# Optimization experiments

Hardware: AMD Instinct MI355X
Metric: run time of the kernel (lower is better)

## Reference

```python
import jax, jax.numpy as jnp
import numpy as np

VOCAB = 128000
HID = 256
SEQ = 512

def setup_inputs() -> dict:
    key = jax.random.key(0)
    k1, k2, k3, k4 = jax.random.split(key, 4)
    input_question = jax.random.randint(k1, (SEQ,), 0, VOCAB, dtype=jnp.int32)
    emb = jax.random.normal(k2, (VOCAB, HID), dtype=jnp.float32) * 0.02
    # torch Linear(2H, H): weight [H, 2H], bias [H]
    W = jax.random.normal(k3, (HID, 2 * HID), dtype=jnp.float32) * (1.0 / np.sqrt(2 * HID))
    b = jax.random.normal(k4, (HID,), dtype=jnp.float32) * 0.01
    return {"input_question": input_question, "emb": emb, "W": W, "b": b}

def reference(input_question, emb, W, b):
    # gather all word embeddings up-front: [S, H]
    xs = emb[input_question]
    # split W into hidden part and input part so each step is two small GEMVs
    Wh = W[:, :HID]   # acts on hidden_state (first in concat)
    Wx = W[:, HID:]   # acts on embedded word
    # precompute input contribution for all steps: [S, H]
    inp = xs @ Wx.T + b

    def step(h, inp_t):
        h_new = jnp.tanh(h @ Wh.T + inp_t)
        return h_new, None

    h0 = jnp.zeros((HID,), dtype=emb.dtype)
    h_final, _ = jax.lax.scan(step, h0, inp)
    return h_final
```

## Files before the change

### kernel.cpp

```cpp
#include <hip/hip_runtime.h>
#include <math.h>

#define HID 256
#define SEQ 512

typedef float v4f __attribute__((ext_vector_type(4)));

__global__ __launch_bounds__(256) void qrnn_phase1(
    const int* __restrict__ idx, const float* __restrict__ emb,
    const float* __restrict__ W, const float* __restrict__ b,
    float* __restrict__ inp)
{
    const int t = blockIdx.x;
    const int i = threadIdx.x;
    __shared__ float xs[HID];
    const size_t row = (size_t)idx[t];
    xs[i] = emb[row * HID + i];
    __syncthreads();

    const float* wr = W + (size_t)i * (2 * HID) + HID;
    float acc = b[i];
#pragma unroll
    for (int k = 0; k < HID / 4; ++k) {
        const float4 w4 = *reinterpret_cast<const float4*>(wr + k * 4);
        const float4 x4 = *reinterpret_cast<const float4*>(&xs[k * 4]);
        acc = fmaf(w4.x, x4.x, acc);
        acc = fmaf(w4.y, x4.y, acc);
        acc = fmaf(w4.z, x4.z, acc);
        acc = fmaf(w4.w, x4.w, acc);
    }
    inp[t * HID + i] = acc;
}

template <int CTRL>
__device__ __forceinline__ float dpp_add(float v)
{
    int x = __builtin_amdgcn_update_dpp(0, __float_as_int(v), CTRL, 0xF, 0xF, true);
    return v + __int_as_float(x);
}

#define PIN8(a) asm volatile("" : "+v"(a[0]), "+v"(a[1]), "+v"(a[2]), \
                                  "+v"(a[3]), "+v"(a[4]), "+v"(a[5]), \
                                  "+v"(a[6]), "+v"(a[7]))

__global__ __launch_bounds__(512, 2) void qrnn_phase2(
    const float* __restrict__ W, const float* __restrict__ inp,
    float* __restrict__ out)
{
    const int tid = threadIdx.x;
    const int r = tid & 7;
    const int g = tid >> 3;
    const int m_out = r & 3;
    const int i_out = 4 * g + m_out;

    __shared__ float hbuf[2][HID];

    if (tid < HID) hbuf[0][tid] = 0.0f;

    v4f wv[4][8];
#pragma unroll
    for (int m = 0; m < 4; ++m) {
        const float* wrow = W + (size_t)(4 * g + m) * (2 * HID) + r * 32;
#pragma unroll
        for (int k = 0; k < 8; ++k)
            wv[m][k] = *reinterpret_cast<const v4f*>(wrow + k * 4);
    }
    PIN8(wv[0]); PIN8(wv[1]); PIN8(wv[2]); PIN8(wv[3]);

    float ip = inp[i_out];
    float h = 0.0f;
    __syncthreads();

    auto step = [&](const float* __restrict__ src, float* __restrict__ dst,
                    int tnext) {
        v4f h4[8];
#pragma unroll
        for (int k = 0; k < 8; ++k)
            h4[k] = *reinterpret_cast<const v4f*>(src + r * 32 + (((k ^ r) & 7) << 2));

        float ip_next = inp[(tnext & (SEQ - 1)) * HID + i_out];

        float acc[4];
#pragma unroll
        for (int m = 0; m < 4; ++m) {
            float a = 0.0f;
#pragma unroll
            for (int k = 0; k < 8; ++k) {
                a = fmaf(wv[m][k].x, h4[k].x, a);
                a = fmaf(wv[m][k].y, h4[k].y, a);
                a = fmaf(wv[m][k].z, h4[k].z, a);
                a = fmaf(wv[m][k].w, h4[k].w, a);
            }
            acc[m] = a;
        }

#pragma unroll
        for (int m = 0; m < 4; ++m) {
            acc[m] = dpp_add<0xB1>(acc[m]);
            acc[m] = dpp_add<0x4E>(acc[m]);
            acc[m] = dpp_add<0x141>(acc[m]);
        }

        float s0 = (r & 1) ? acc[1] : acc[0];
        float s1 = (r & 1) ? acc[3] : acc[2];
        float d  = (r & 2) ? s1 : s0;

        d += ip;
        float e = __expf(2.0f * d);
        h = 1.0f - 2.0f / (e + 1.0f);

        if (r < 4)
            dst[i_out ^ (((i_out >> 5) & 7) << 2)] = h;

        ip = ip_next;
        __syncthreads();
    };

#pragma unroll 1
    for (int t = 0; t < SEQ; t += 2) {
        step(&hbuf[0][0], &hbuf[1][0], t + 1);
        step(&hbuf[1][0], &hbuf[0][0], t + 2);
    }

    if (r < 4) out[i_out] = h;
}

extern "C" void kernel_launch(void* const* d_in, const int* in_sizes, int n_in,
                              void* d_out, int out_size, void* d_ws, size_t ws_size,
                              hipStream_t stream)
{
    const int*   idx = (const int*)d_in[0];
    const float* emb = (const float*)d_in[1];
    const float* W   = (const float*)d_in[2];
    const float* b   = (const float*)d_in[3];
    float* out = (float*)d_out;
    float* inp = (float*)d_ws;

    qrnn_phase1<<<SEQ, HID, 0, stream>>>(idx, emb, W, b, inp);
    qrnn_phase2<<<1, 512, 0, stream>>>(W, inp, out);
}
```

Baseline: 281.2 us.

## Repartition recurrent GEMV to 16 lanes per 8 rows with butterfly reduce-scatter

Phase 2 now assigns 16 lanes to each group of 8 output rows, so each lane covers 16 columns instead of 32. The cross-lane reduction becomes a recursive-halving reduce-scatter using DPP moves with select-based give/keep, which replaces the full all-reduce on every accumulator. The goal is to shorten the serial FMA chain and cut DPP/add work per step on the sequential critical path. In exchange it adds row-rotate DPP controls and more select logic, and drops the minimum-blocks hint in favour of a waves_per_eu attribute.

```diff
diff --git a/kernel.cpp b/kernel.cpp
--- a/kernel.cpp
+++ b/kernel.cpp
@@ -33,39 +33,49 @@
 }
 
 template <int CTRL>
-__device__ __forceinline__ float dpp_add(float v)
+__device__ __forceinline__ float dpp_mov(float v)
 {
-    int x = __builtin_amdgcn_update_dpp(0, __float_as_int(v), CTRL, 0xF, 0xF, true);
-    return v + __int_as_float(x);
+    return __int_as_float(
+        __builtin_amdgcn_update_dpp(0, __float_as_int(v), CTRL, 0xF, 0xF, true));
 }
 
-#define PIN8(a) asm volatile("" : "+v"(a[0]), "+v"(a[1]), "+v"(a[2]), \
-                                  "+v"(a[3]), "+v"(a[4]), "+v"(a[5]), \
-                                  "+v"(a[6]), "+v"(a[7]))
+#define PIN4(a) asm volatile("" : "+v"(a[0]), "+v"(a[1]), "+v"(a[2]), "+v"(a[3]))
 
-__global__ __launch_bounds__(512, 2) void qrnn_phase2(
-    const float* __restrict__ W, const float* __restrict__ inp,
-    float* __restrict__ out)
+__global__ void __launch_bounds__(512)
+__attribute__((amdgpu_waves_per_eu(2, 2)))
+qrnn_phase2(const float* __restrict__ W, const float* __restrict__ inp,
+            float* __restrict__ out)
 {
     const int tid = threadIdx.x;
-    const int r = tid & 7;
-    const int g = tid >> 3;
-    const int m_out = r & 3;
-    const int i_out = 4 * g + m_out;
+    const int r = tid & 15;
+    const int g = tid >> 4;
+    const bool b0 = (r & 1) != 0;
+    const bool b1 = (r & 2) != 0;
+    const bool b2 = (r & 4) != 0;
+    const bool b3 = (r & 8) != 0;
+    const int m_r = (r & 3) | ((r >> 1) & 4);
+    const int i_out = 8 * g + m_r;
 
     __shared__ float hbuf[2][HID];
-
     if (tid < HID) hbuf[0][tid] = 0.0f;
 
-    v4f wv[4][8];
+    v4f wv[8][4];
 #pragma unroll
-    for (int m = 0; m < 4; ++m) {
-        const float* wrow = W + (size_t)(4 * g + m) * (2 * HID) + r * 32;
+    for (int m = 0; m < 8; ++m) {
+        const float* wrow = W + (size_t)(8 * g + m) * (2 * HID) + r * 16;
 #pragma unroll
-        for (int k = 0; k < 8; ++k)
+        for (int k = 0; k < 4; ++k)
             wv[m][k] = *reinterpret_cast<const v4f*>(wrow + k * 4);
+        PIN4(wv[m]);
     }
-    PIN8(wv[0]); PIN8(wv[1]); PIN8(wv[2]); PIN8(wv[3]);
+
+    int rdoff[4];
+#pragma unroll
+    for (int k = 0; k < 4; ++k) {
+        const int w = 16 * r + 4 * k;
+        rdoff[k] = w ^ (((w >> 5) & 7) << 2);
+    }
+    const int wroff = i_out ^ (((i_out >> 5) & 7) << 2);
 
     float ip = inp[i_out];
     float h = 0.0f;
@@ -73,19 +83,19 @@
 
     auto step = [&](const float* __restrict__ src, float* __restrict__ dst,
                     int tnext) {
-        v4f h4[8];
+        v4f h4[4];
 #pragma unroll
-        for (int k = 0; k < 8; ++k)
-            h4[k] = *reinterpret_cast<const v4f*>(src + r * 32 + (((k ^ r) & 7) << 2));
+        for (int k = 0; k < 4; ++k)
+            h4[k] = *reinterpret_cast<const v4f*>(src + rdoff[k]);
 
         float ip_next = inp[(tnext & (SEQ - 1)) * HID + i_out];
 
-        float acc[4];
+        float acc[8];
 #pragma unroll
-        for (int m = 0; m < 4; ++m) {
+        for (int m = 0; m < 8; ++m) {
             float a = 0.0f;
 #pragma unroll
-            for (int k = 0; k < 8; ++k) {
+            for (int k = 0; k < 4; ++k) {
                 a = fmaf(wv[m][k].x, h4[k].x, a);
                 a = fmaf(wv[m][k].y, h4[k].y, a);
                 a = fmaf(wv[m][k].z, h4[k].z, a);
@@ -94,23 +104,32 @@
             acc[m] = a;
         }
 
+        float q[4];
 #pragma unroll
-        for (int m = 0; m < 4; ++m) {
-            acc[m] = dpp_add<0xB1>(acc[m]);
-            acc[m] = dpp_add<0x4E>(acc[m]);
-            acc[m] = dpp_add<0x141>(acc[m]);
+        for (int j = 0; j < 4; ++j) {
+            float give = b0 ? acc[2 * j] : acc[2 * j + 1];
+            float keep = b0 ? acc[2 * j + 1] : acc[2 * j];
+            q[j] = keep + dpp_mov<0xB1>(give);
         }
+        float s2[2];
+#pragma unroll
+        for (int k2 = 0; k2 < 2; ++k2) {
+            float give = b1 ? q[2 * k2] : q[2 * k2 + 1];
+            float keep = b1 ? q[2 * k2 + 1] : q[2 * k2];
+            s2[k2] = keep + dpp_mov<0x4E>(give);
+        }
+        float give3 = b3 ? s2[0] : s2[1];
+        float keep3 = b3 ? s2[1] : s2[0];
+        float ssum = keep3 + dpp_mov<0x128>(give3);
+        float a4  = dpp_mov<0x124>(ssum);
+        float a12 = dpp_mov<0x12C>(ssum);
+        float total = ssum + (b2 ? a4 : a12);
 
-        float s0 = (r & 1) ? acc[1] : acc[0];
-        float s1 = (r & 1) ? acc[3] : acc[2];
-        float d  = (r & 2) ? s1 : s0;
-
-        d += ip;
+        float d = total + ip;
         float e = __expf(2.0f * d);
         h = 1.0f - 2.0f / (e + 1.0f);
 
-        if (r < 4)
-            dst[i_out ^ (((i_out >> 5) & 7) << 2)] = h;
+        if (!b2) dst[wroff] = h;
 
         ip = ip_next;
         __syncthreads();
@@ -122,7 +141,7 @@
         step(&hbuf[1][0], &hbuf[0][0], t + 2);
     }
 
-    if (r < 4) out[i_out] = h;
+    if (!b2) out[i_out] = h;
 }
 
 extern "C" void kernel_launch(void* const* d_in, const int* in_sizes, int n_in,
```

New measurement: 291.7 us. 3.7% more time.

## Use fp16 MFMA for recurrent hidden-state GEMV with weights pinned in AGPRs

Applied to the files above, without the earlier changes.

Rewrites the sequential recurrence kernel so each step's Wh·h product runs on MFMA 16x16x32 f16 instructions. Wh is converted to fp16 and held in accumulator registers, and the hidden state is exchanged through fp16 shared memory. This removes the per-step scalar FMA chain and DPP reductions and cuts the block to 256 threads. MFMA is used as a matrix-vector product by broadcasting h across columns, which wastes most of the MFMA throughput and adds MFMA latency on the serial path. Rounding weights and hidden state to fp16 lowers precision across 512 recurrent steps.

```diff
diff --git a/kernel.cpp b/kernel.cpp
--- a/kernel.cpp
+++ b/kernel.cpp
@@ -4,7 +4,9 @@
 #define HID 256
 #define SEQ 512
 
-typedef float v4f __attribute__((ext_vector_type(4)));
+typedef _Float16 half8 __attribute__((ext_vector_type(8)));
+typedef _Float16 half4 __attribute__((ext_vector_type(4)));
+typedef float    f32x4 __attribute__((ext_vector_type(4)));
 
 __global__ __launch_bounds__(256) void qrnn_phase1(
     const int* __restrict__ idx, const float* __restrict__ emb,
@@ -32,87 +34,84 @@
     inp[t * HID + i] = acc;
 }
 
-template <int CTRL>
-__device__ __forceinline__ float dpp_add(float v)
-{
-    int x = __builtin_amdgcn_update_dpp(0, __float_as_int(v), CTRL, 0xF, 0xF, true);
-    return v + __int_as_float(x);
-}
+#define PIN_A(x) asm volatile("" : "+a"(x))
 
-#define PIN8(a) asm volatile("" : "+v"(a[0]), "+v"(a[1]), "+v"(a[2]), \
-                                  "+v"(a[3]), "+v"(a[4]), "+v"(a[5]), \
-                                  "+v"(a[6]), "+v"(a[7]))
-
-__global__ __launch_bounds__(512, 2) void qrnn_phase2(
+__global__ __launch_bounds__(256) void qrnn_phase2(
     const float* __restrict__ W, const float* __restrict__ inp,
     float* __restrict__ out)
 {
-    const int tid = threadIdx.x;
-    const int r = tid & 7;
-    const int g = tid >> 3;
-    const int m_out = r & 3;
-    const int i_out = 4 * g + m_out;
+    const int tid  = threadIdx.x;
+    const int wave = tid >> 6;
+    const int l    = tid & 63;
+    const int c    = l & 15;
+    const int q    = l >> 4;
+    const int rbase = 64 * wave;
 
-    __shared__ float hbuf[2][HID];
+    __shared__ __align__(16) _Float16 hbuf[2][HID];
+    hbuf[0][tid] = (_Float16)0.0f;
 
-    if (tid < HID) hbuf[0][tid] = 0.0f;
+    half8 af[4][8];
+#pragma unroll
+    for (int rt = 0; rt < 4; ++rt) {
+#pragma unroll
+        for (int kc = 0; kc < 8; ++kc) {
+            const float* wr =
+                W + (size_t)(rbase + 16 * rt + c) * (2 * HID) + 32 * kc + 8 * q;
+            half8 v;
+#pragma unroll
+            for (int j = 0; j < 8; ++j) v[j] = (_Float16)wr[j];
+            af[rt][kc] = v;
+            PIN_A(af[rt][kc]);
+        }
+    }
 
-    v4f wv[4][8];
-#pragma unroll
-    for (int m = 0; m < 4; ++m) {
-        const float* wrow = W + (size_t)(4 * g + m) * (2 * HID) + r * 32;
-#pragma unroll
-        for (int k = 0; k < 8; ++k)
-            wv[m][k] = *reinterpret_cast<const v4f*>(wrow + k * 4);
-    }
-    PIN8(wv[0]); PIN8(wv[1]); PIN8(wv[2]); PIN8(wv[3]);
+    const int iprow = rbase + 16 * (c & 3) + 4 * q;
+    f32x4 ipv = *reinterpret_cast<const f32x4*>(inp + iprow);
 
-    float ip = inp[i_out];
-    float h = 0.0f;
+    f32x4 hout = {0.0f, 0.0f, 0.0f, 0.0f};
     __syncthreads();
 
-    auto step = [&](const float* __restrict__ src, float* __restrict__ dst,
-                    int tnext) {
-        v4f h4[8];
+    auto step = [&](const _Float16* __restrict__ src,
+                    _Float16* __restrict__ dst, int tnext) {
+        half8 bf[8];
 #pragma unroll
-        for (int k = 0; k < 8; ++k)
-            h4[k] = *reinterpret_cast<const v4f*>(src + r * 32 + (((k ^ r) & 7) << 2));
+        for (int kc = 0; kc < 8; ++kc)
+            bf[kc] = *reinterpret_cast<const half8*>(src + 32 * kc + 8 * q);
 
-        float ip_next = inp[(tnext & (SEQ - 1)) * HID + i_out];
+        f32x4 ip_next = *reinterpret_cast<const f32x4*>(
+            inp + (size_t)(tnext & (SEQ - 1)) * HID + iprow);
 
-        float acc[4];
+        f32x4 acc[4];
 #pragma unroll
-        for (int m = 0; m < 4; ++m) {
-            float a = 0.0f;
+        for (int rt = 0; rt < 4; ++rt) acc[rt] = (f32x4){0.f, 0.f, 0.f, 0.f};
 #pragma unroll
-            for (int k = 0; k < 8; ++k) {
-                a = fmaf(wv[m][k].x, h4[k].x, a);
-                a = fmaf(wv[m][k].y, h4[k].y, a);
-                a = fmaf(wv[m][k].z, h4[k].z, a);
-                a = fmaf(wv[m][k].w, h4[k].w, a);
-            }
-            acc[m] = a;
+        for (int kc = 0; kc < 8; ++kc) {
+#pragma unroll
+            for (int rt = 0; rt < 4; ++rt)
+                acc[rt] = __builtin_amdgcn_mfma_f32_16x16x32_f16(
+                    af[rt][kc], bf[kc], acc[rt], 0, 0, 0);
         }
 
+        f32x4 m01 = (c & 1) ? acc[1] : acc[0];
+        f32x4 m23 = (c & 1) ? acc[3] : acc[2];
+        f32x4 mine = (c & 2) ? m23 : m01;
+
+        f32x4 d = mine + ipv;
+        f32x4 hN;
 #pragma unroll
-        for (int m = 0; m < 4; ++m) {
-            acc[m] = dpp_add<0xB1>(acc[m]);
-            acc[m] = dpp_add<0x4E>(acc[m]);
-            acc[m] = dpp_add<0x141>(acc[m]);
+        for (int j = 0; j < 4; ++j) {
+            float e = __expf(2.0f * d[j]);
+            hN[j] = 1.0f - 2.0f / (e + 1.0f);
+        }
+        hout = hN;
+
+        if (c < 4) {
+            half4 hh = { (_Float16)hN[0], (_Float16)hN[1],
+                         (_Float16)hN[2], (_Float16)hN[3] };
+            *reinterpret_cast<half4*>(dst + rbase + 16 * c + 4 * q) = hh;
         }
 
-        float s0 = (r & 1) ? acc[1] : acc[0];
-        float s1 = (r & 1) ? acc[3] : acc[2];
-        float d  = (r & 2) ? s1 : s0;
-
-        d += ip;
-        float e = __expf(2.0f * d);
-        h = 1.0f - 2.0f / (e + 1.0f);
-
-        if (r < 4)
-            dst[i_out ^ (((i_out >> 5) & 7) << 2)] = h;
-
-        ip = ip_next;
+        ipv = ip_next;
         __syncthreads();
     };
 
@@ -122,7 +121,10 @@
         step(&hbuf[1][0], &hbuf[0][0], t + 2);
     }
 
-    if (r < 4) out[i_out] = h;
+    if (c < 4) {
+        *reinterpret_cast<float4*>(out + rbase + 16 * c + 4 * q) =
+            (float4){ hout[0], hout[1], hout[2], hout[3] };
+    }
 }
 
 extern "C" void kernel_launch(void* const* d_in, const int* in_sizes, int n_in,
@@ -137,5 +139,5 @@
     float* inp = (float*)d_ws;
 
     qrnn_phase1<<<SEQ, HID, 0, stream>>>(idx, emb, W, b, inp);
-    qrnn_phase2<<<1, 512, 0, stream>>>(W, inp, out);
+    qrnn_phase2<<<1, 256, 0, stream>>>(W, inp, out);
 }
```

New measurement: 309.1 us. +9.9%, slower.
